# Kernel optimization log

Hardware: AMD Instinct MI355X
Metric: run time of the kernel (lower is better)

Reference implementation:

```python
import jax, jax.numpy as jnp
import numpy as np

W1 = 7          # half window
W2 = 2 * W1 + 1 # window size = 15
H = 4           # num heads
DH = 64         # head dim
DO = H * DH     # 256


def setup_inputs() -> dict:
    key = jax.random.key(0)
    ks = jax.random.split(key, 7)
    B, T, D = 2, 4096, 768
    s = 1.0 / np.sqrt(D).astype(np.float32)
    inputs = jax.random.normal(ks[0], (B, T, D), dtype=jnp.float32)
    Wq = jax.random.normal(ks[1], (DO, D), dtype=jnp.float32) * s
    bq = jax.random.normal(ks[2], (DO,), dtype=jnp.float32) * s
    Wv = jax.random.normal(ks[3], (DO, D), dtype=jnp.float32) * s
    bv = jax.random.normal(ks[4], (DO,), dtype=jnp.float32) * s
    pos_emb = jax.random.normal(ks[5], (W2, D), dtype=jnp.float32)
    return {"inputs": inputs, "Wq": Wq, "bq": bq, "Wv": Wv, "bv": bv, "pos_emb": pos_emb}


def reference(inputs, Wq, bq, Wv, bv, pos_emb):
    # Faithful to the torch module: k uses the *query* projection (source bug),
    # no softmax, no 1/sqrt(d) scaling.
    B, T, D = inputs.shape
    pad = jnp.pad(inputs, ((0, 0), (W1, W1), (0, 0)))  # [B, T+2*W1, D]
    # Project once on the padded sequence, then gather windows (linear ops
    # commute with the window gather; position bias added post-projection).
    q_pad = pad @ Wq.T + bq            # [B, T+2*W1, DO]
    v_pad = pad @ Wv.T + bv            # [B, T+2*W1, DO]
    pos_q = pos_emb @ Wq.T             # [W2, DO]  (query(window+pos) = query(window)+pos@Wq^T)
    pos_v = pos_emb @ Wv.T             # [W2, DO]
    idx = jnp.arange(T)[:, None] + jnp.arange(W2)[None, :]  # [T, W2]
    k = q_pad[:, idx] + pos_q          # [B, T, W2, DO]
    v = v_pad[:, idx] + pos_v          # [B, T, W2, DO]
    q = inputs @ Wq.T + bq             # [B, T, DO]
    qh = q.reshape(B, T, H, DH)
    kh = k.reshape(B, T, W2, H, DH)
    vh = v.reshape(B, T, W2, H, DH)
    scores = jnp.einsum('bthd,btwhd->bthw', qh, kh)   # [B, T, H, W2] (no softmax)
    ctx = jnp.einsum('bthw,btwhd->bthd', scores, vh)  # [B, T, H, DH]
    return ctx.reshape(B, T, DO)
```

## Files before the change

kernel.cpp:

```cpp
#include <hip/hip_runtime.h>

#define TPC   4110
#define MROWS 8220
#define MTOT  8235
#define MPAD  8320
#define KD    768

typedef __attribute__((ext_vector_type(8))) short short8;
typedef __attribute__((ext_vector_type(4))) float f32x4;

#define LOAD_LDS16(gp, lp)                                                   \
  __builtin_amdgcn_global_load_lds(                                          \
      (const __attribute__((address_space(1))) void*)(gp),                   \
      (__attribute__((address_space(3))) void*)(lp), 16, 0, 0)

__device__ inline unsigned bfr(float x) {
  unsigned u = __float_as_uint(x);
  return (u + 0x7FFFu + ((u >> 16) & 1u)) >> 16;
}
__device__ inline unsigned pack2(float a, float b) {
  return bfr(a) | (bfr(b) << 16);
}
__device__ inline float bflo(unsigned u) { return __uint_as_float(u << 16); }
__device__ inline float bfhi(unsigned u) { return __uint_as_float(u & 0xffff0000u); }

__global__ __launch_bounds__(256) void cast_ab(
    const float* __restrict__ inp, const float* __restrict__ Wq,
    const float* __restrict__ Wv, const float* __restrict__ pos,
    ushort* __restrict__ Abf, ushort* __restrict__ Wbf) {
  const int ACH = MPAD * 96;
  int gid = blockIdx.x * 256 + threadIdx.x;
  const float* src = nullptr;
  ushort* dst;
  if (gid < ACH) {
    int row = gid / 96, c = (gid - row * 96) * 8;
    dst = Abf + (size_t)row * KD + c;
    if (row < MROWS) {
      int b = row / TPC, t = row - b * TPC - 7;
      if (t >= 0 && t < 4096) src = inp + ((size_t)b * 4096 + t) * KD + c;
    } else if (row < MTOT) {
      src = pos + (size_t)(row - MROWS) * KD + c;
    }
  } else {
    int wid = gid - ACH;
    if (wid >= 512 * 96) return;
    int row = wid / 96, c = (wid - row * 96) * 8;
    dst = Wbf + (size_t)row * KD + c;
    src = (row < 256) ? Wq + (size_t)row * KD + c
                      : Wv + (size_t)(row - 256) * KD + c;
  }
  uint4 o;
  if (src) {
    float4 f0 = *(const float4*)src;
    float4 f1 = *(const float4*)(src + 4);
    o.x = pack2(f0.x, f0.y); o.y = pack2(f0.z, f0.w);
    o.z = pack2(f1.x, f1.y); o.w = pack2(f1.z, f1.w);
  } else {
    o.x = o.y = o.z = o.w = 0u;
  }
  *(uint4*)dst = o;
}

__global__ __launch_bounds__(256) void gemm_bf16(
    const ushort* __restrict__ Abf, const ushort* __restrict__ Wbf,
    const float* __restrict__ bq, const float* __restrict__ bv,
    ushort* __restrict__ q_out, ushort* __restrict__ v_out,
    ushort* __restrict__ pos_q, ushort* __restrict__ pos_v) {
  __shared__ ushort Al[64 * 32];
  __shared__ ushort Bl[128 * 32];
  const int tid = threadIdx.x;
  const int wave = tid >> 6, lane = tid & 63;
  const int ns = blockIdx.x;
  const int m0 = blockIdx.y * 64;
  const int wm = wave & 1, wn = wave >> 1;
  const int fr = lane & 15, quad = lane >> 4;

  const int srow = tid >> 2, skc = (tid & 3) * 8;
  const ushort* ag  = Abf + (size_t)(m0 + srow) * KD + skc;
  const ushort* bg0 = Wbf + (size_t)(ns * 128 + srow) * KD + skc;
  const ushort* bg1 = bg0 + (size_t)64 * KD;
  ushort* al  = Al + wave * 512;
  ushort* bl0 = Bl + wave * 512;
  ushort* bl1 = Bl + 2048 + wave * 512;

  f32x4 acc[2][4];
  #pragma unroll
  for (int i = 0; i < 2; i++)
    #pragma unroll
    for (int j = 0; j < 4; j++) acc[i][j] = 0.0f;

  for (int k0 = 0; k0 < KD; k0 += 32) {
    LOAD_LDS16(ag + k0, al);
    LOAD_LDS16(bg0 + k0, bl0);
    LOAD_LDS16(bg1 + k0, bl1);
    __syncthreads();
    short8 af[2], bf[4];
    #pragma unroll
    for (int i = 0; i < 2; i++)
      af[i] = *(const short8*)(Al + (wm * 32 + i * 16 + fr) * 32 + quad * 8);
    #pragma unroll
    for (int j = 0; j < 4; j++)
      bf[j] = *(const short8*)(Bl + (wn * 64 + j * 16 + fr) * 32 + quad * 8);
    #pragma unroll
    for (int i = 0; i < 2; i++)
      #pragma unroll
      for (int j = 0; j < 4; j++)
        acc[i][j] = __builtin_amdgcn_mfma_f32_16x16x32_bf16(af[i], bf[j],
                                                            acc[i][j], 0, 0, 0);
    __syncthreads();
  }

  const float* bias = (ns < 2) ? bq : bv;
  ushort* outp = (ns < 2) ? q_out : v_out;
  ushort* posp = (ns < 2) ? pos_q : pos_v;
  const int wbase = (ns & 1) * 128;
  #pragma unroll
  for (int j = 0; j < 4; j++) {
    const int colq = wbase + wn * 64 + j * 16 + fr;
    const int h = colq >> 6, d = colq & 63;
    const float bj = bias[colq];
    #pragma unroll
    for (int i = 0; i < 2; i++) {
      const int mb = m0 + wm * 32 + i * 16 + quad * 4;
      #pragma unroll
      for (int r = 0; r < 4; r++) {
        const int m = mb + r;
        if (m < MROWS) {
          int b = m / TPC, tp = m - b * TPC;
          outp[(((size_t)(b * 4 + h)) * TPC + tp) * 64 + d] =
              (ushort)bfr(acc[i][j][r] + bj);
        } else if (m < MTOT) {
          posp[(m - MROWS) * 256 + colq] = (ushort)bfr(acc[i][j][r]);
        }
      }
    }
  }
}

__global__ __launch_bounds__(256) void win_attn4(
    const ushort* __restrict__ q_out, const ushort* __restrict__ v_out,
    const ushort* __restrict__ pos_q, const ushort* __restrict__ pos_v,
    float* __restrict__ out) {
  __shared__ __align__(16) float ks[78][68];
  __shared__ __align__(16) float vs[78][68];
  __shared__ __align__(16) float pq[15][68];
  __shared__ __align__(16) float pv[15][68];
  const int tid = threadIdx.x;
  const int bh = blockIdx.x >> 6, tile = blockIdx.x & 63;
  const int b = bh >> 2, h = bh & 3;
  const int t0 = tile * 64;

  const size_t slab = (((size_t)(b * 4 + h)) * TPC + t0) * 64;
  for (int idx = tid; idx < 624; idx += 256) {
    int row = idx >> 3, c8 = (idx & 7) * 8;
    uint4 kc = *(const uint4*)(q_out + slab + idx * 8);
    ks[row][c8 + 0] = bflo(kc.x); ks[row][c8 + 1] = bfhi(kc.x);
    ks[row][c8 + 2] = bflo(kc.y); ks[row][c8 + 3] = bfhi(kc.y);
    ks[row][c8 + 4] = bflo(kc.z); ks[row][c8 + 5] = bfhi(kc.z);
    ks[row][c8 + 6] = bflo(kc.w); ks[row][c8 + 7] = bfhi(kc.w);
    uint4 vc = *(const uint4*)(v_out + slab + idx * 8);
    vs[row][c8 + 0] = bflo(vc.x); vs[row][c8 + 1] = bfhi(vc.x);
    vs[row][c8 + 2] = bflo(vc.y); vs[row][c8 + 3] = bfhi(vc.y);
    vs[row][c8 + 4] = bflo(vc.z); vs[row][c8 + 5] = bfhi(vc.z);
    vs[row][c8 + 6] = bflo(vc.w); vs[row][c8 + 7] = bfhi(vc.w);
  }
  if (tid < 120) {
    int row = tid >> 3, c8 = (tid & 7) * 8;
    uint4 qc = *(const uint4*)(pos_q + row * 256 + h * 64 + c8);
    pq[row][c8 + 0] = bflo(qc.x); pq[row][c8 + 1] = bfhi(qc.x);
    pq[row][c8 + 2] = bflo(qc.y); pq[row][c8 + 3] = bfhi(qc.y);
    pq[row][c8 + 4] = bflo(qc.z); pq[row][c8 + 5] = bfhi(qc.z);
    pq[row][c8 + 6] = bflo(qc.w); pq[row][c8 + 7] = bfhi(qc.w);
    uint4 vc = *(const uint4*)(pos_v + row * 256 + h * 64 + c8);
    pv[row][c8 + 0] = bflo(vc.x); pv[row][c8 + 1] = bfhi(vc.x);
    pv[row][c8 + 2] = bflo(vc.y); pv[row][c8 + 3] = bfhi(vc.y);
    pv[row][c8 + 4] = bflo(vc.z); pv[row][c8 + 5] = bfhi(vc.z);
    pv[row][c8 + 6] = bflo(vc.w); pv[row][c8 + 7] = bfhi(vc.w);
  }
  __syncthreads();

  const int tl = tid >> 2, qtr = tid & 3, d0 = qtr * 16;
  float4 qv[4];
  #pragma unroll
  for (int c = 0; c < 4; c++) qv[c] = *(float4*)&ks[tl + 7][d0 + c * 4];
  float4 ctx[4];
  #pragma unroll
  for (int c = 0; c < 4; c++) ctx[c] = make_float4(0.f, 0.f, 0.f, 0.f);

  #pragma unroll
  for (int w = 0; w < 15; w++) {
    float p = 0.f;
    #pragma unroll
    for (int c = 0; c < 4; c++) {
      float4 kk = *(float4*)&ks[tl + w][d0 + c * 4];
      float4 pp = *(float4*)&pq[w][d0 + c * 4];
      p += qv[c].x * (kk.x + pp.x) + qv[c].y * (kk.y + pp.y) +
           qv[c].z * (kk.z + pp.z) + qv[c].w * (kk.w + pp.w);
    }
    p += __shfl_xor(p, 1, 64);
    p += __shfl_xor(p, 2, 64);
    #pragma unroll
    for (int c = 0; c < 4; c++) {
      float4 vv = *(float4*)&vs[tl + w][d0 + c * 4];
      float4 pp = *(float4*)&pv[w][d0 + c * 4];
      ctx[c].x += p * (vv.x + pp.x);
      ctx[c].y += p * (vv.y + pp.y);
      ctx[c].z += p * (vv.z + pp.z);
      ctx[c].w += p * (vv.w + pp.w);
    }
  }
  size_t oo = ((size_t)(b * 4096 + t0 + tl)) * 256 + h * 64 + d0;
  #pragma unroll
  for (int c = 0; c < 4; c++) *(float4*)(out + oo + c * 4) = ctx[c];
}

extern "C" void kernel_launch(void* const* d_in, const int* in_sizes, int n_in,
                              void* d_out, int out_size, void* d_ws,
                              size_t ws_size, hipStream_t stream) {
  const float* inp = (const float*)d_in[0];
  const float* Wq  = (const float*)d_in[1];
  const float* bq  = (const float*)d_in[2];
  const float* Wv  = (const float*)d_in[3];
  const float* bv  = (const float*)d_in[4];
  const float* pos = (const float*)d_in[5];
  float* out = (float*)d_out;

  char* ws = (char*)d_ws;
  ushort* Abf   = (ushort*)ws;
  ushort* Wbf   = (ushort*)(ws + 12779520);
  ushort* q_out = (ushort*)(ws + 13565952);
  ushort* v_out = (ushort*)(ws + 17774592);
  ushort* pos_q = (ushort*)(ws + 21983232);
  ushort* pos_v = (ushort*)(ws + 21990912);

  const int cast_chunks = MPAD * 96 + 512 * 96;
  hipLaunchKernelGGL(cast_ab, dim3(cast_chunks / 256), dim3(256), 0, stream,
                     inp, Wq, Wv, pos, Abf, Wbf);
  hipLaunchKernelGGL(gemm_bf16, dim3(4, MPAD / 64), dim3(256), 0, stream,
                     Abf, Wbf, bq, bv, q_out, v_out, pos_q, pos_v);
  hipLaunchKernelGGL(win_attn4, dim3(2 * 4 * 64), dim3(256), 0, stream,
                     q_out, v_out, pos_q, pos_v, out);
}
```

Measured before the change: 113.1 us.

## Double GEMM K-tile to 64 with XOR-swizzled LDS layout

Raises the K step of the bf16 projection GEMM from 32 to 64, so each iteration loads twice as much data into LDS and halves the number of barrier pairs. The global addresses are XOR-swizzled by row so that the fragment reads from LDS avoid bank conflicts at the wider 64-element row stride. This doubles LDS use per block, which may reduce occupancy, and adds swizzle index arithmetic.

```diff
diff --git a/kernel.cpp b/kernel.cpp
--- a/kernel.cpp
+++ b/kernel.cpp
@@ -66,8 +66,8 @@
     const float* __restrict__ bq, const float* __restrict__ bv,
     ushort* __restrict__ q_out, ushort* __restrict__ v_out,
     ushort* __restrict__ pos_q, ushort* __restrict__ pos_v) {
-  __shared__ ushort Al[64 * 32];
-  __shared__ ushort Bl[128 * 32];
+  __shared__ ushort Al[64 * 64];
+  __shared__ ushort Bl[128 * 64];
   const int tid = threadIdx.x;
   const int wave = tid >> 6, lane = tid & 63;
   const int ns = blockIdx.x;
@@ -75,13 +75,24 @@
   const int wm = wave & 1, wn = wave >> 1;
   const int fr = lane & 15, quad = lane >> 4;
 
-  const int srow = tid >> 2, skc = (tid & 3) * 8;
-  const ushort* ag  = Abf + (size_t)(m0 + srow) * KD + skc;
-  const ushort* bg0 = Wbf + (size_t)(ns * 128 + srow) * KD + skc;
-  const ushort* bg1 = bg0 + (size_t)64 * KD;
-  ushort* al  = Al + wave * 512;
-  ushort* bl0 = Bl + wave * 512;
-  ushort* bl1 = Bl + 2048 + wave * 512;
+  const ushort* ag[2];
+  #pragma unroll
+  for (int i = 0; i < 2; i++) {
+    int c = i * 256 + tid, row = c >> 3, kq = c & 7;
+    ag[i] = Abf + (size_t)(m0 + row) * KD + ((kq ^ (row & 7)) * 8);
+  }
+  const ushort* bg[4];
+  #pragma unroll
+  for (int i = 0; i < 4; i++) {
+    int c = i * 256 + tid, row = c >> 3, kq = c & 7;
+    bg[i] = Wbf + (size_t)(ns * 128 + row) * KD + ((kq ^ (row & 7)) * 8);
+  }
+  ushort* al[2];
+  ushort* bl[4];
+  #pragma unroll
+  for (int i = 0; i < 2; i++) al[i] = Al + (i * 256 + wave * 64) * 8;
+  #pragma unroll
+  for (int i = 0; i < 4; i++) bl[i] = Bl + (i * 256 + wave * 64) * 8;
 
   f32x4 acc[2][4];
   #pragma unroll
@@ -89,24 +100,31 @@
     #pragma unroll
     for (int j = 0; j < 4; j++) acc[i][j] = 0.0f;
 
-  for (int k0 = 0; k0 < KD; k0 += 32) {
-    LOAD_LDS16(ag + k0, al);
-    LOAD_LDS16(bg0 + k0, bl0);
-    LOAD_LDS16(bg1 + k0, bl1);
+  for (int k0 = 0; k0 < KD; k0 += 64) {
+    #pragma unroll
+    for (int i = 0; i < 2; i++) LOAD_LDS16(ag[i] + k0, al[i]);
+    #pragma unroll
+    for (int i = 0; i < 4; i++) LOAD_LDS16(bg[i] + k0, bl[i]);
     __syncthreads();
-    short8 af[2], bf[4];
-    #pragma unroll
-    for (int i = 0; i < 2; i++)
-      af[i] = *(const short8*)(Al + (wm * 32 + i * 16 + fr) * 32 + quad * 8);
-    #pragma unroll
-    for (int j = 0; j < 4; j++)
-      bf[j] = *(const short8*)(Bl + (wn * 64 + j * 16 + fr) * 32 + quad * 8);
-    #pragma unroll
-    for (int i = 0; i < 2; i++)
+    short8 af[2][2], bf[2][4];
+    #pragma unroll
+    for (int ks = 0; ks < 2; ks++) {
+      const int e = ((ks * 4 + quad) ^ (fr & 7)) * 8;
+      #pragma unroll
+      for (int i = 0; i < 2; i++)
+        af[ks][i] = *(const short8*)(Al + (wm * 32 + i * 16 + fr) * 64 + e);
       #pragma unroll
       for (int j = 0; j < 4; j++)
-        acc[i][j] = __builtin_amdgcn_mfma_f32_16x16x32_bf16(af[i], bf[j],
-                                                            acc[i][j], 0, 0, 0);
+        bf[ks][j] = *(const short8*)(Bl + (wn * 64 + j * 16 + fr) * 64 + e);
+    }
+    #pragma unroll
+    for (int ks = 0; ks < 2; ks++)
+      #pragma unroll
+      for (int i = 0; i < 2; i++)
+        #pragma unroll
+        for (int j = 0; j < 4; j++)
+          acc[i][j] = __builtin_amdgcn_mfma_f32_16x16x32_bf16(
+              af[ks][i], bf[ks][j], acc[i][j], 0, 0, 0);
     __syncthreads();
   }
 
```

Result: faster. 109.6 us (median of 2 runs) (-3.1%).
